# Kernel optimization log

Measured on AMD Instinct MI355X. Metric: run time of the kernel, lower is better.

Reference implementation:

```python
import jax, jax.numpy as jnp
import numpy as np
import math

D_MODEL = 1024
N_HEADS = 16
D_K = D_MODEL // N_HEADS
THETA = 0.1


def setup_inputs() -> dict:
    key = jax.random.key(0)
    ks = jax.random.split(key, 6)
    scale = np.sqrt(1.0 / D_MODEL).astype(np.float32)
    x = jax.random.normal(ks[0], (4, 2048, D_MODEL), dtype=jnp.float32)
    W_q = jax.random.normal(ks[1], (D_MODEL, D_MODEL), dtype=jnp.float32) * scale
    W_k = jax.random.normal(ks[2], (D_MODEL, D_MODEL), dtype=jnp.float32) * scale
    W_v = jax.random.normal(ks[3], (D_MODEL, D_MODEL), dtype=jnp.float32) * scale
    W_o = jax.random.normal(ks[4], (D_MODEL, D_MODEL), dtype=jnp.float32) * scale
    alpha = jnp.ones((1,), dtype=jnp.float32)
    return {"x": x, "W_q": W_q, "W_k": W_k, "W_v": W_v, "W_o": W_o, "alpha": alpha}


def reference(x, W_q, W_k, W_v, W_o, alpha):
    B, S, _ = x.shape
    Q = x @ W_q
    K = x @ W_k
    V = x @ W_v
    # non-commutative elementwise transforms
    Q = Q + THETA * jnp.sin(Q)
    K = K + THETA * jnp.cos(K)
    V = V + alpha * THETA * jnp.tanh(V)
    # split heads: [B, H, S, d_k]
    def split(t):
        return t.reshape(B, S, N_HEADS, D_K).transpose(0, 2, 1, 3)
    Qh, Kh, Vh = split(Q), split(K), split(V)
    scores = jnp.einsum('bhqd,bhkd->bhqk', Qh, Kh) / math.sqrt(D_K)
    attn = jax.nn.softmax(scores, axis=-1)
    out = jnp.einsum('bhqk,bhkd->bhqd', attn, Vh)
    out = out.transpose(0, 2, 1, 3).reshape(B, S, D_MODEL)
    return out @ W_o
```

## Files before the change

### kernel.cpp

```cpp
#include <hip/hip_runtime.h>

typedef __bf16 bf16x8 __attribute__((ext_vector_type(8)));
typedef float f32x4 __attribute__((ext_vector_type(4)));
typedef float f32x16 __attribute__((ext_vector_type(16)));

#define MFMA16(a,b,c) __builtin_amdgcn_mfma_f32_16x16x32_bf16(a,b,c,0,0,0)
#define MFMA32(a,b,c) __builtin_amdgcn_mfma_f32_32x32x16_bf16(a,b,c,0,0,0)

__device__ __forceinline__ unsigned short f2bf(float f) {
  unsigned int u = __float_as_uint(f);
  u = (u + 0x7FFFu + ((u >> 16) & 1u)) >> 16;
  return (unsigned short)u;
}

__device__ __forceinline__ void gload16(const void* g, void* l) {
  __builtin_amdgcn_global_load_lds(
      (const __attribute__((address_space(1))) void*)g,
      (__attribute__((address_space(3))) void*)l, 16, 0, 0);
}

__device__ __forceinline__ float vexp2(float x) {
  float r;
  asm("v_exp_f32 %0, %1" : "=v"(r) : "v"(x));
  return r;
}

__device__ __forceinline__ bf16x8 mk_pfrag(int hi, float p0, float p1, float p2, float p3,
                                           float p4, float p5, float p6, float p7) {
  unsigned int a0, a1, b0, b1;
  asm("v_cvt_pk_bf16_f32 %0, %1, %2" : "=v"(a0) : "v"(p0), "v"(p1));
  asm("v_cvt_pk_bf16_f32 %0, %1, %2" : "=v"(a1) : "v"(p2), "v"(p3));
  asm("v_cvt_pk_bf16_f32 %0, %1, %2" : "=v"(b0) : "v"(p4), "v"(p5));
  asm("v_cvt_pk_bf16_f32 %0, %1, %2" : "=v"(b1) : "v"(p6), "v"(p7));
  unsigned int x = __shfl_xor(hi ? a0 : b0, 32);
  unsigned int y = __shfl_xor(hi ? a1 : b1, 32);
  uint4 w;
  w.x = hi ? x : a0;
  w.y = hi ? y : a1;
  w.z = hi ? b0 : x;
  w.w = hi ? b1 : y;
  return *reinterpret_cast<bf16x8*>(&w);
}

__global__ __launch_bounds__(256) void k_convx(const float* __restrict__ x,
                                               unsigned short* __restrict__ xb) {
  int i = (blockIdx.x * 256 + threadIdx.x) * 4;
  float4 v = *reinterpret_cast<const float4*>(x + i);
  ushort4 o;
  o.x = f2bf(v.x); o.y = f2bf(v.y); o.z = f2bf(v.z); o.w = f2bf(v.w);
  *reinterpret_cast<ushort4*>(xb + i) = o;
}

__global__ __launch_bounds__(256) void k_transw(const float* __restrict__ W,
                                                unsigned short* __restrict__ WT) {
  __shared__ float t[32][33];
  int bx = blockIdx.x * 32;
  int by = blockIdx.y * 32;
  int tx = threadIdx.x & 31;
  int ty = threadIdx.x >> 5;
#pragma unroll
  for (int i = 0; i < 32; i += 8)
    t[ty + i][tx] = W[(size_t)(by + ty + i) * 1024 + bx + tx];
  __syncthreads();
#pragma unroll
  for (int i = 0; i < 32; i += 8)
    WT[(size_t)(bx + ty + i) * 1024 + by + tx] = f2bf(t[tx][ty + i]);
}

template <int EPI>
__global__ __launch_bounds__(256) void k_gemm(
    const unsigned short* __restrict__ A, const unsigned short* __restrict__ BT, int K,
    unsigned short* __restrict__ Qf, unsigned short* __restrict__ Kf,
    unsigned short* __restrict__ VT, const float* __restrict__ alphaPtr,
    float* __restrict__ Out) {
  __shared__ __align__(16) unsigned short smem[128 * 136];
  unsigned short* AsBase = smem;
  unsigned short* BsBase = smem + 128 * 32;
  const int tid = threadIdx.x;
  const int wave = tid >> 6, lane = tid & 63;
  const int l15 = lane & 15, lg = lane >> 4;
  const int wr = wave >> 1, wc = wave & 1;
  const int bm = blockIdx.x, bn = blockIdx.y;

  f32x4 acc[4][4] = {};
  const unsigned short* Ab = A + (size_t)bm * 128 * K;
  const unsigned short* Bb = BT + (size_t)bn * 128 * K;

  const int r0 = tid >> 2, q0 = (tid & 3) * 8;
  const int r1 = r0 + 64;
  char* ldsA = (char*)AsBase + wave * 1024;
  char* ldsB = (char*)BsBase + wave * 1024;

  for (int k0 = 0; k0 < K; k0 += 32) {
    gload16((const void*)(Ab + (size_t)r0 * K + k0 + q0), ldsA);
    gload16((const void*)(Ab + (size_t)r1 * K + k0 + q0), ldsA + 4096);
    gload16((const void*)(Bb + (size_t)r0 * K + k0 + q0), ldsB);
    gload16((const void*)(Bb + (size_t)r1 * K + k0 + q0), ldsB + 4096);
    __syncthreads();
    bf16x8 af[4], bfr[4];
#pragma unroll
    for (int mi = 0; mi < 4; ++mi)
      af[mi] = *reinterpret_cast<const bf16x8*>(&AsBase[(wr * 64 + mi * 16 + l15) * 32 + lg * 8]);
#pragma unroll
    for (int ni = 0; ni < 4; ++ni)
      bfr[ni] = *reinterpret_cast<const bf16x8*>(&BsBase[(wc * 64 + ni * 16 + l15) * 32 + lg * 8]);
#pragma unroll
    for (int mi = 0; mi < 4; ++mi)
#pragma unroll
      for (int ni = 0; ni < 4; ++ni)
        acc[mi][ni] = MFMA16(af[mi], bfr[ni], acc[mi][ni]);
    __syncthreads();
  }

  if (EPI == 0) {
    const float av = alphaPtr[0];
    const int t = bn >> 3;
    if (t == 2) {
#pragma unroll
      for (int mi = 0; mi < 4; ++mi) {
        int row0 = bm * 128 + wr * 64 + mi * 16 + lg * 4;
        int bb = row0 >> 11, s = row0 & 2047;
#pragma unroll
        for (int ni = 0; ni < 4; ++ni) {
          int col = (bn & 7) * 128 + wc * 64 + ni * 16 + l15;
          int hh = col >> 6, dd = col & 63;
          ushort4 pk;
#pragma unroll
          for (int r = 0; r < 4; ++r) {
            float v = acc[mi][ni][r];
            float e = __expf(2.0f * v);
            v += av * 0.1f * (1.0f - 2.0f * __builtin_amdgcn_rcpf(e + 1.0f));
            ((unsigned short*)&pk)[r] = f2bf(v);
          }
          *reinterpret_cast<ushort4*>(VT + ((size_t)(bb * 16 + hh) * 64 + dd) * 2048 + s) = pk;
        }
      }
    } else {
#pragma unroll
      for (int mi = 0; mi < 4; ++mi)
#pragma unroll
        for (int ni = 0; ni < 4; ++ni)
#pragma unroll
          for (int r = 0; r < 4; ++r) {
            int row = wr * 64 + mi * 16 + lg * 4 + r;
            int col = wc * 64 + ni * 16 + l15;
            float v = acc[mi][ni][r];
            if (t == 0) v += 0.1f * __sinf(v);
            else v += 0.1f * __cosf(v);
            smem[row * 136 + col] = f2bf(v);
          }
      __syncthreads();
      unsigned short* dst = (t == 0) ? Qf : Kf;
      const int c16 = tid & 15, rb = tid >> 4;
      const int ncol0 = (bn & 7) * 128;
#pragma unroll
      for (int i2 = 0; i2 < 8; ++i2) {
        int srow = rb + i2 * 16;
        uint4 val = *reinterpret_cast<const uint4*>(&smem[srow * 136 + c16 * 8]);
        *reinterpret_cast<uint4*>(dst + (size_t)(bm * 128 + srow) * 1024 + ncol0 + c16 * 8) = val;
      }
    }
  } else {
#pragma unroll
    for (int ni = 0; ni < 4; ++ni) {
      int n = bn * 128 + wc * 64 + ni * 16 + l15;
#pragma unroll
      for (int mi = 0; mi < 4; ++mi) {
        int row = bm * 128 + wr * 64 + mi * 16 + lg * 4;
#pragma unroll
        for (int r = 0; r < 4; ++r)
          Out[(size_t)(row + r) * 1024 + n] = acc[mi][ni][r];
      }
    }
  }
}

__global__ __launch_bounds__(256)
void k_attn(const unsigned short* __restrict__ Qf,
            const unsigned short* __restrict__ Kf,
            const unsigned short* __restrict__ VT,
            unsigned short* __restrict__ AO) {
  __shared__ __align__(16) unsigned short smem[2 * 8192];
  const int tid = threadIdx.x;
  const int wave = tid >> 6, lane = tid & 63;
  const int l31 = lane & 31, hi = lane >> 5;
  const int f = (blockIdx.y << 4) | blockIdx.x;
  const int nf = ((f & 7) << 7) | (f >> 3);
  const int qb = nf & 15, bh = nf >> 4;
  const int b = bh >> 4, h = bh & 15;

  const unsigned short* Qb = Qf + ((size_t)b * 2048 + qb * 128 + wave * 32) * 1024 + h * 64;
  const unsigned short* Kb = Kf + (size_t)b * 2048 * 1024 + h * 64;
  const unsigned short* Vb = VT + (size_t)bh * 64 * 2048;

  bf16x8 qfr[4];
#pragma unroll
  for (int ds = 0; ds < 4; ++ds)
    qfr[ds] = *reinterpret_cast<const bf16x8*>(Qb + (size_t)l31 * 1024 + ds * 16 + hi * 8);

  float lsum = 0.f;
  f32x16 o0 = {}, o1 = {};

  const int krow0 = wave * 16 + (lane >> 3);
  const int ksrcc = ((lane & 7) ^ (lane >> 3)) << 3;
  const int kxor = l31 & 7;

  const float C1 = 0.18033688011112042f;

  {
    gload16((const void*)(Kb + (size_t)krow0 * 1024 + ksrcc), (char*)smem + wave * 2048);
    gload16((const void*)(Kb + (size_t)(krow0 + 8) * 1024 + ksrcc), (char*)smem + wave * 2048 + 1024);
    gload16((const void*)(Vb + (size_t)krow0 * 2048 + ksrcc), (char*)(smem + 4096) + wave * 2048);
    gload16((const void*)(Vb + (size_t)(krow0 + 8) * 2048 + ksrcc),
            (char*)(smem + 4096) + wave * 2048 + 1024);
  }
  __syncthreads();

  for (int t = 0; t < 32; ++t) {
    unsigned short* KsC = smem + (t & 1) * 8192;
    unsigned short* VTC = KsC + 4096;
    unsigned short* KsN = smem + ((t + 1) & 1) * 8192;
    unsigned short* VTN = KsN + 4096;

    if (t < 31) {
      int kn = (t + 1) * 64;
      gload16((const void*)(Kb + (size_t)(kn + krow0) * 1024 + ksrcc), (char*)KsN + wave * 2048);
      gload16((const void*)(Kb + (size_t)(kn + krow0 + 8) * 1024 + ksrcc),
              (char*)KsN + wave * 2048 + 1024);
      gload16((const void*)(Vb + (size_t)krow0 * 2048 + kn + ksrcc), (char*)VTN + wave * 2048);
      gload16((const void*)(Vb + (size_t)(krow0 + 8) * 2048 + kn + ksrcc),
              (char*)VTN + wave * 2048 + 1024);
    }

    f32x16 s0 = {}, s1 = {};
    __builtin_amdgcn_s_setprio(1);
#pragma unroll
    for (int ds = 0; ds < 4; ++ds) {
      int ch = ((ds * 2 + hi) ^ kxor) * 8;
      bf16x8 kf0 = *reinterpret_cast<const bf16x8*>(&KsC[l31 * 64 + ch]);
      bf16x8 kf1 = *reinterpret_cast<const bf16x8*>(&KsC[(l31 + 32) * 64 + ch]);
      s0 = MFMA32(kf0, qfr[ds], s0);
      s1 = MFMA32(kf1, qfr[ds], s1);
    }
    __builtin_amdgcn_s_setprio(0);

    float rs0 = 0.f, rs1 = 0.f, rs2 = 0.f, rs3 = 0.f;
#pragma unroll
    for (int r = 0; r < 16; r += 4) {
      float p0 = vexp2(s0[r] * C1);     s0[r] = p0;     rs0 += p0;
      float p1 = vexp2(s0[r + 1] * C1); s0[r + 1] = p1; rs1 += p1;
      float p2 = vexp2(s0[r + 2] * C1); s0[r + 2] = p2; rs2 += p2;
      float p3 = vexp2(s0[r + 3] * C1); s0[r + 3] = p3; rs3 += p3;
    }
#pragma unroll
    for (int r = 0; r < 16; r += 4) {
      float p0 = vexp2(s1[r] * C1);     s1[r] = p0;     rs0 += p0;
      float p1 = vexp2(s1[r + 1] * C1); s1[r + 1] = p1; rs1 += p1;
      float p2 = vexp2(s1[r + 2] * C1); s1[r + 2] = p2; rs2 += p2;
      float p3 = vexp2(s1[r + 3] * C1); s1[r + 3] = p3; rs3 += p3;
    }
    lsum += (rs0 + rs1) + (rs2 + rs3);

    __builtin_amdgcn_s_setprio(1);
#pragma unroll
    for (int ks = 0; ks < 4; ++ks) {
      bf16x8 pf =
          (ks == 0) ? mk_pfrag(hi, s0[0], s0[1], s0[2], s0[3], s0[4], s0[5], s0[6], s0[7])
        : (ks == 1) ? mk_pfrag(hi, s0[8], s0[9], s0[10], s0[11], s0[12], s0[13], s0[14], s0[15])
        : (ks == 2) ? mk_pfrag(hi, s1[0], s1[1], s1[2], s1[3], s1[4], s1[5], s1[6], s1[7])
                    : mk_pfrag(hi, s1[8], s1[9], s1[10], s1[11], s1[12], s1[13], s1[14], s1[15]);
      int ch = ((ks * 2 + hi) ^ kxor) * 8;
      bf16x8 v0 = *reinterpret_cast<const bf16x8*>(&VTC[l31 * 64 + ch]);
      bf16x8 v1 = *reinterpret_cast<const bf16x8*>(&VTC[(l31 + 32) * 64 + ch]);
      o0 = MFMA32(v0, pf, o0);
      o1 = MFMA32(v1, pf, o1);
    }
    __builtin_amdgcn_s_setprio(0);
    __syncthreads();
  }

  lsum += __shfl_xor(lsum, 32);
  const float inv = 1.0f / lsum;
  unsigned short* OL = smem + wave * 2304;
#pragma unroll
  for (int r = 0; r < 16; ++r) {
    int d0 = (r & 3) + 8 * (r >> 2) + 4 * hi;
    OL[l31 * 72 + d0] = f2bf(o0[r] * inv);
    OL[l31 * 72 + 32 + d0] = f2bf(o1[r] * inv);
  }
  __syncthreads();
#pragma unroll
  for (int p = 0; p < 4; ++p) {
    int u = tid + p * 256;
    int row = u >> 3, ch = u & 7;
    uint4 val = *reinterpret_cast<const uint4*>(&smem[(row >> 5) * 2304 + (row & 31) * 72 + ch * 8]);
    *reinterpret_cast<uint4*>(AO + ((size_t)b * 2048 + qb * 128 + row) * 1024 + h * 64 + ch * 8) = val;
  }
}

extern "C" void kernel_launch(void* const* d_in, const int* in_sizes, int n_in,
                              void* d_out, int out_size, void* d_ws, size_t ws_size,
                              hipStream_t stream) {
  const float* x = (const float*)d_in[0];
  const float* Wq = (const float*)d_in[1];
  const float* Wk = (const float*)d_in[2];
  const float* Wv = (const float*)d_in[3];
  const float* Wo = (const float*)d_in[4];
  const float* alpha = (const float*)d_in[5];
  float* out = (float*)d_out;

  char* ws = (char*)d_ws;
  unsigned short* xb  = (unsigned short*)(ws);
  unsigned short* WT3 = (unsigned short*)(ws + 16777216);
  unsigned short* WoT = (unsigned short*)(ws + 23068672);
  unsigned short* Qf  = (unsigned short*)(ws + 25165824);
  unsigned short* Kf  = (unsigned short*)(ws + 41943040);
  unsigned short* VTb = (unsigned short*)(ws + 58720256);
  unsigned short* AO  = (unsigned short*)(ws + 75497472);

  k_convx<<<dim3(8192), dim3(256), 0, stream>>>(x, xb);
  k_transw<<<dim3(32, 32), dim3(256), 0, stream>>>(Wq, WT3);
  k_transw<<<dim3(32, 32), dim3(256), 0, stream>>>(Wk, WT3 + 1024 * 1024);
  k_transw<<<dim3(32, 32), dim3(256), 0, stream>>>(Wv, WT3 + 2 * 1024 * 1024);
  k_transw<<<dim3(32, 32), dim3(256), 0, stream>>>(Wo, WoT);

  k_gemm<0><<<dim3(64, 24), dim3(256), 0, stream>>>(xb, WT3, 1024, Qf, Kf, VTb, alpha, nullptr);
  k_attn<<<dim3(16, 64), dim3(256), 0, stream>>>(Qf, Kf, VTb, AO);
  k_gemm<1><<<dim3(64, 8), dim3(256), 0, stream>>>(AO, WoT, 1024, nullptr, nullptr, nullptr, nullptr, out);
}
```

Measured before the change: 230.0 us.

## Triple-buffer K/V tiles in attention and fold softmax scale into Q

The attention kernel moves from double to triple buffering of K/V tiles in LDS. It prefetches two tiles ahead, waits with explicit vmcnt counters, and uses a single barrier per iteration instead of a trailing __syncthreads. This is meant to hide global load latency behind the MFMA and exp work. Separately, the softmax scale (log2e/sqrt(dk)) is multiplied into Q in the projection epilogue, which removes a multiply per score element; the catch is that Q is now rounded to bf16 after scaling, which shifts rounding slightly. LDS use goes up by half, which may reduce occupancy.

```diff
diff --git a/kernel.cpp b/kernel.cpp
--- a/kernel.cpp
+++ b/kernel.cpp
@@ -145,8 +145,12 @@
             int row = wr * 64 + mi * 16 + lg * 4 + r;
             int col = wc * 64 + ni * 16 + l15;
             float v = acc[mi][ni][r];
-            if (t == 0) v += 0.1f * __sinf(v);
-            else v += 0.1f * __cosf(v);
+            if (t == 0) {
+              v += 0.1f * __sinf(v);
+              v *= 0.18033688011112042f;
+            } else {
+              v += 0.1f * __cosf(v);
+            }
             smem[row * 136 + col] = f2bf(v);
           }
       __syncthreads();
@@ -180,7 +184,7 @@
             const unsigned short* __restrict__ Kf,
             const unsigned short* __restrict__ VT,
             unsigned short* __restrict__ AO) {
-  __shared__ __align__(16) unsigned short smem[2 * 8192];
+  __shared__ __align__(16) unsigned short smem[3 * 8192];
   const int tid = threadIdx.x;
   const int wave = tid >> 6, lane = tid & 63;
   const int l31 = lane & 31, hi = lane >> 5;
@@ -197,6 +201,7 @@
 #pragma unroll
   for (int ds = 0; ds < 4; ++ds)
     qfr[ds] = *reinterpret_cast<const bf16x8*>(Qb + (size_t)l31 * 1024 + ds * 16 + hi * 8);
+  asm volatile("s_waitcnt vmcnt(0)" ::: "memory");
 
   float lsum = 0.f;
   f32x16 o0 = {}, o1 = {};
@@ -205,31 +210,34 @@
   const int ksrcc = ((lane & 7) ^ (lane >> 3)) << 3;
   const int kxor = l31 & 7;
 
-  const float C1 = 0.18033688011112042f;
-
-  {
-    gload16((const void*)(Kb + (size_t)krow0 * 1024 + ksrcc), (char*)smem + wave * 2048);
-    gload16((const void*)(Kb + (size_t)(krow0 + 8) * 1024 + ksrcc), (char*)smem + wave * 2048 + 1024);
-    gload16((const void*)(Vb + (size_t)krow0 * 2048 + ksrcc), (char*)(smem + 4096) + wave * 2048);
-    gload16((const void*)(Vb + (size_t)(krow0 + 8) * 2048 + ksrcc),
-            (char*)(smem + 4096) + wave * 2048 + 1024);
-  }
-  __syncthreads();
+#pragma unroll
+  for (int tt = 0; tt < 2; ++tt) {
+    char* Kd = (char*)(smem + tt * 8192) + wave * 2048;
+    char* Vd = (char*)(smem + tt * 8192 + 4096) + wave * 2048;
+    int kn = tt * 64;
+    gload16((const void*)(Kb + (size_t)(kn + krow0) * 1024 + ksrcc), Kd);
+    gload16((const void*)(Kb + (size_t)(kn + krow0 + 8) * 1024 + ksrcc), Kd + 1024);
+    gload16((const void*)(Vb + (size_t)krow0 * 2048 + kn + ksrcc), Vd);
+    gload16((const void*)(Vb + (size_t)(krow0 + 8) * 2048 + kn + ksrcc), Vd + 1024);
+  }
 
   for (int t = 0; t < 32; ++t) {
-    unsigned short* KsC = smem + (t & 1) * 8192;
-    unsigned short* VTC = KsC + 4096;
-    unsigned short* KsN = smem + ((t + 1) & 1) * 8192;
-    unsigned short* VTN = KsN + 4096;
-
-    if (t < 31) {
-      int kn = (t + 1) * 64;
-      gload16((const void*)(Kb + (size_t)(kn + krow0) * 1024 + ksrcc), (char*)KsN + wave * 2048);
-      gload16((const void*)(Kb + (size_t)(kn + krow0 + 8) * 1024 + ksrcc),
-              (char*)KsN + wave * 2048 + 1024);
-      gload16((const void*)(Vb + (size_t)krow0 * 2048 + kn + ksrcc), (char*)VTN + wave * 2048);
-      gload16((const void*)(Vb + (size_t)(krow0 + 8) * 2048 + kn + ksrcc),
-              (char*)VTN + wave * 2048 + 1024);
+    const unsigned short* KsC = smem + (t % 3) * 8192;
+    const unsigned short* VTC = KsC + 4096;
+
+    if (t < 31) asm volatile("s_waitcnt vmcnt(4)" ::: "memory");
+    else        asm volatile("s_waitcnt vmcnt(0)" ::: "memory");
+    __builtin_amdgcn_s_barrier();
+    __builtin_amdgcn_sched_barrier(0);
+
+    if (t < 30) {
+      int kn = (t + 2) * 64;
+      char* Kd = (char*)(smem + ((t + 2) % 3) * 8192) + wave * 2048;
+      char* Vd = (char*)(smem + ((t + 2) % 3) * 8192 + 4096) + wave * 2048;
+      gload16((const void*)(Kb + (size_t)(kn + krow0) * 1024 + ksrcc), Kd);
+      gload16((const void*)(Kb + (size_t)(kn + krow0 + 8) * 1024 + ksrcc), Kd + 1024);
+      gload16((const void*)(Vb + (size_t)krow0 * 2048 + kn + ksrcc), Vd);
+      gload16((const void*)(Vb + (size_t)(krow0 + 8) * 2048 + kn + ksrcc), Vd + 1024);
     }
 
     f32x16 s0 = {}, s1 = {};
@@ -247,17 +255,17 @@
     float rs0 = 0.f, rs1 = 0.f, rs2 = 0.f, rs3 = 0.f;
 #pragma unroll
     for (int r = 0; r < 16; r += 4) {
-      float p0 = vexp2(s0[r] * C1);     s0[r] = p0;     rs0 += p0;
-      float p1 = vexp2(s0[r + 1] * C1); s0[r + 1] = p1; rs1 += p1;
-      float p2 = vexp2(s0[r + 2] * C1); s0[r + 2] = p2; rs2 += p2;
-      float p3 = vexp2(s0[r + 3] * C1); s0[r + 3] = p3; rs3 += p3;
+      float p0 = vexp2(s0[r]);     s0[r] = p0;     rs0 += p0;
+      float p1 = vexp2(s0[r + 1]); s0[r + 1] = p1; rs1 += p1;
+      float p2 = vexp2(s0[r + 2]); s0[r + 2] = p2; rs2 += p2;
+      float p3 = vexp2(s0[r + 3]); s0[r + 3] = p3; rs3 += p3;
     }
 #pragma unroll
     for (int r = 0; r < 16; r += 4) {
-      float p0 = vexp2(s1[r] * C1);     s1[r] = p0;     rs0 += p0;
-      float p1 = vexp2(s1[r + 1] * C1); s1[r + 1] = p1; rs1 += p1;
-      float p2 = vexp2(s1[r + 2] * C1); s1[r + 2] = p2; rs2 += p2;
-      float p3 = vexp2(s1[r + 3] * C1); s1[r + 3] = p3; rs3 += p3;
+      float p0 = vexp2(s1[r]);     s1[r] = p0;     rs0 += p0;
+      float p1 = vexp2(s1[r + 1]); s1[r + 1] = p1; rs1 += p1;
+      float p2 = vexp2(s1[r + 2]); s1[r + 2] = p2; rs2 += p2;
+      float p3 = vexp2(s1[r + 3]); s1[r + 3] = p3; rs3 += p3;
     }
     lsum += (rs0 + rs1) + (rs2 + rs3);
 
@@ -276,8 +284,8 @@
       o1 = MFMA32(v1, pf, o1);
     }
     __builtin_amdgcn_s_setprio(0);
-    __syncthreads();
-  }
+  }
+  __syncthreads();
 
   lsum += __shfl_xor(lsum, 32);
   const float inv = 1.0f / lsum;
```

Result: no change. 226.2 us (-1.7%).
